# Optimization experiments

Measured on AMD Instinct MI355X. Metric: run time of the kernel, lower is better.

Reference implementation:

```python
import jax, jax.numpy as jnp
import numpy as np
from jax import lax

NUM_WORD, NUM_TAG, EMB, HID, SEQ = 50000, 50, 500, 200, 4096
START, END = 48, 49
NEG = -10000.0


def setup_inputs() -> dict:
    key = jax.random.key(0)
    ks = jax.random.split(key, 16)
    s = 0.1  # weight scale for numerical sanity
    trans = jax.random.normal(ks[13], (NUM_TAG, NUM_TAG), jnp.float32)
    trans = trans.at[START, :].set(NEG).at[:, END].set(NEG)
    return {
        'sentence_ids': jax.random.randint(ks[0], (1, SEQ), 0, NUM_WORD),
        'tags_ids': jax.random.randint(ks[1], (SEQ,), 0, START),
        'embedding': jax.random.normal(ks[2], (NUM_WORD, EMB), jnp.float32),
        'w_ih_f': s * jax.random.normal(ks[3], (4 * HID, EMB), jnp.float32),
        'w_hh_f': s * jax.random.normal(ks[4], (4 * HID, HID), jnp.float32),
        'b_ih_f': s * jax.random.normal(ks[5], (4 * HID,), jnp.float32),
        'b_hh_f': s * jax.random.normal(ks[6], (4 * HID,), jnp.float32),
        'w_ih_b': s * jax.random.normal(ks[7], (4 * HID, EMB), jnp.float32),
        'w_hh_b': s * jax.random.normal(ks[8], (4 * HID, HID), jnp.float32),
        'b_ih_b': s * jax.random.normal(ks[9], (4 * HID,), jnp.float32),
        'b_hh_b': s * jax.random.normal(ks[10], (4 * HID,), jnp.float32),
        'linear_w': s * jax.random.normal(ks[11], (NUM_TAG, 2 * HID), jnp.float32),
        'linear_b': s * jax.random.normal(ks[12], (NUM_TAG,), jnp.float32),
        'transitions': trans,
        'h0': jax.random.normal(ks[14], (2, HID), jnp.float32),
        'c0': jax.random.normal(ks[15], (2, HID), jnp.float32),
    }


def _lstm_dir(x_proj, w_hh, h0, c0):
    # x_proj: [S, 4H] precomputed input projection (+ both biases)
    def step(carry, xp):
        h, c = carry
        g = xp + h @ w_hh.T  # [4H], torch gate order i,f,g,o
        i, f, gg, o = jnp.split(g, 4)
        c = jax.nn.sigmoid(f) * c + jax.nn.sigmoid(i) * jnp.tanh(gg)
        h = jax.nn.sigmoid(o) * jnp.tanh(c)
        return (h, c), h
    _, hs = lax.scan(step, (h0, c0), x_proj)
    return hs  # [S, H]


def _get_feats(sentence_ids, embedding, w_ih_f, w_hh_f, b_ih_f, b_hh_f,
               w_ih_b, w_hh_b, b_ih_b, b_hh_b, linear_w, linear_b, h0, c0):
    x = embedding[sentence_ids[0]]  # [S, EMB]
    xf = x @ w_ih_f.T + (b_ih_f + b_hh_f)  # one big GEMM, fold hh-bias in
    xb = x[::-1] @ w_ih_b.T + (b_ih_b + b_hh_b)
    hf = _lstm_dir(xf, w_hh_f, h0[0], c0[0])          # [S, H]
    hb = _lstm_dir(xb, w_hh_b, h0[1], c0[1])[::-1]    # [S, H]
    h = jnp.concatenate([hf, hb], axis=-1)            # [S, 2H]
    return h @ linear_w.T + linear_b                   # [S, NUM_TAG]


def _crf_forward(feats, transitions):
    alpha = jnp.full((NUM_TAG,), NEG, feats.dtype).at[START].set(0.0)
    def step(alpha, feat):
        smat = alpha[:, None] + transitions + feat[None, :]  # [T, T]
        return jax.nn.logsumexp(smat, axis=0), None
    alpha, _ = lax.scan(step, alpha, feats)
    return jax.nn.logsumexp(alpha + transitions[:, END])


def _gold_score(feats, tags_ids, transitions):
    tags = jnp.concatenate([jnp.array([START], tags_ids.dtype), tags_ids])
    trans_sc = transitions[tags[:-1], tags[1:]].sum()
    emit_sc = feats[jnp.arange(feats.shape[0]), tags[1:]].sum()
    return trans_sc + emit_sc + transitions[tags[-1], END]


def _viterbi(feats, transitions):
    alpha = jnp.full((NUM_TAG,), NEG, feats.dtype).at[START].set(0.0)
    def step(alpha, feat):
        smat = alpha[:, None] + feat[None, :] + transitions  # [T, T]
        return smat.max(axis=0), smat.argmax(axis=0)
    alpha, bp = lax.scan(step, alpha, feats)  # bp: [S, T]
    fin = alpha + transitions[:, END]
    best = jnp.argmax(fin)
    def bt(tag, bp_t):
        prev = bp_t[tag]
        return prev, prev
    _, prevs = lax.scan(bt, best, bp[1:][::-1])  # skip first frame, as torch
    path = jnp.concatenate([prevs[::-1], best[None]])  # [S]
    return fin[best], path


def reference(sentence_ids, tags_ids, embedding, w_ih_f, w_hh_f, b_ih_f, b_hh_f,
              w_ih_b, w_hh_b, b_ih_b, b_hh_b, linear_w, linear_b, transitions,
              h0, c0):
    feats = _get_feats(sentence_ids, embedding, w_ih_f, w_hh_f, b_ih_f, b_hh_f,
                       w_ih_b, w_hh_b, b_ih_b, b_hh_b, linear_w, linear_b, h0, c0)
    fwd_score = _crf_forward(feats, transitions)
    gold = _gold_score(feats, tags_ids, transitions)
    _, tag_seq = _viterbi(feats, transitions)
    loss = jnp.reshape(fwd_score - gold, (1,))
    return (tag_seq, loss)
```

## Files before the change

### kernel.cpp

```cpp
#include <hip/hip_runtime.h>

typedef unsigned int u32;
typedef unsigned char u8;

#define TSTART 48
#define TEND   49
#define NEGV  -10000.0f

#define O_XG     0ull
#define O_WIHF   4194304ull
#define O_WIHB   5013504ull
#define O_WHHF   5832704ull
#define O_WHHB   6193152ull
#define O_BSF    6553600ull
#define O_BSB    6556800ull
#define O_LWP    6560000ull
#define O_XF     6600000ull
#define O_XB     19707200ull
#define O_HT     32814400ull
#define O_FEATS  36091200ull
#define O_BP     36910400ull
#define O_FMAP   37115200ull
#define O_BTAG   37118400ull
#define O_SCAL   37118656ull

typedef _Float16 h2 __attribute__((ext_vector_type(2)));

__device__ __forceinline__ float fdot2(u32 a, u32 b, float c) {
#if defined(__HIP_DEVICE_COMPILE__) && __has_builtin(__builtin_amdgcn_fdot2)
    return __builtin_amdgcn_fdot2(__builtin_bit_cast(h2, a), __builtin_bit_cast(h2, b), c, false);
#else
    float d;
    asm("v_dot2_f32_f16 %0, %1, %2, %3" : "=v"(d) : "v"(a), "v"(b), "v"(c));
    return d;
#endif
}

__device__ __forceinline__ u32 pack2(float a, float b) {
    u32 lo = __builtin_bit_cast(unsigned short, (_Float16)a);
    u32 hi = __builtin_bit_cast(unsigned short, (_Float16)b);
    return lo | (hi << 16);
}

__device__ __forceinline__ float sigf(float x) { return 1.f / (1.f + __expf(-x)); }
__device__ __forceinline__ float tanhf_(float x) { return 2.f / (1.f + __expf(-2.f * x)) - 1.f; }

#define PA_END   90112
#define PB_END   180224
#define PC_END   385024
#define PD_END   589824
#define PE_END   1638400
#define PF_END   1648400
#define PG_END   1649200
#define PH_END   1650000

__global__ __launch_bounds__(256) void k_prep(
    const int* __restrict__ ids, const float* __restrict__ emb,
    const float* __restrict__ wihf, const float* __restrict__ wihb,
    const float* __restrict__ whhf, const float* __restrict__ whhb,
    const float* __restrict__ bihf, const float* __restrict__ bhhf,
    const float* __restrict__ bihb, const float* __restrict__ bhhb,
    const float* __restrict__ lw,
    u32* __restrict__ xg, u32* __restrict__ wif16, u32* __restrict__ wib16,
    u32* __restrict__ whf16, u32* __restrict__ whb16, u32* __restrict__ lwp,
    float* __restrict__ bsf, float* __restrict__ bsb)
{
    int idx = blockIdx.x * 256 + threadIdx.x;
    if (idx < PB_END) {
        int dirb = (idx >= PA_END);
        int i = idx - (dirb ? PA_END : 0);
        const float* whh = dirb ? whhb : whhf;
        u32* dst = dirb ? whb16 : whf16;
        int chunk = i / 176, off = i % 176;
        int rgrp = chunk >> 2, ks = chunk & 3;
        u32 v = 0;
        if (off < 175) {
            int m, kd;
            if (off < 168) { int q = off >> 2, e = off & 3; kd = ks * 25 + (q / 7) * 4 + e; m = q % 7; }
            else           { m = off - 168; kd = ks * 25 + 24; }
            int row = rgrp * 7 + m;
            if (row < 800) v = pack2(whh[row * 200 + 2 * kd], whh[row * 200 + 2 * kd + 1]);
        }
        dst[i] = v;
    } else if (idx < PD_END) {
        int dirb = (idx >= PC_END);
        int i = idx - (dirb ? PC_END : PB_END);
        const float* wih = dirb ? wihb : wihf;
        u32* dst = dirb ? wib16 : wif16;
        int r = i >> 8, d = i & 255;
        dst[i] = (d < 250) ? pack2(wih[r * 500 + 2 * d], wih[r * 500 + 2 * d + 1]) : 0u;
    } else if (idx < PE_END) {
        int i = idx - PD_END; int s = i >> 8, d = i & 255;
        long id = ids[s];
        xg[i] = (d < 250) ? pack2(emb[id * 500 + 2 * d], emb[id * 500 + 2 * d + 1]) : 0u;
    } else if (idx < PF_END) {
        int i = idx - PE_END; int tag = i / 200, u = i % 200;
        lwp[i] = pack2(lw[tag * 400 + 2 * u], lw[tag * 400 + 2 * u + 1]);
    } else if (idx < PG_END) {
        int j = idx - PF_END; bsf[j] = bihf[j] + bhhf[j];
    } else if (idx < PH_END) {
        int j = idx - PG_END; bsb[j] = bihb[j] + bhhb[j];
    }
}

__global__ __launch_bounds__(256, 2) void k_gemm(
    const u32* __restrict__ xg, const u32* __restrict__ wf, const u32* __restrict__ wb,
    const float* __restrict__ bsf, const float* __restrict__ bsb,
    float* __restrict__ xf, float* __restrict__ xb)
{
    int z = blockIdx.z;
    const u32* W = z ? wb : wf;
    const float* bs = z ? bsb : bsf;
    float* out = z ? xb : xf;
    int m0 = blockIdx.x * 256, n0 = blockIdx.y * 128;
    int t = threadIdx.x;

    __shared__ u32 As[16][256];
    __shared__ u32 Bs[16][128];

    float acc[16][8];
#pragma unroll
    for (int m = 0; m < 16; m++)
#pragma unroll
        for (int n = 0; n < 8; n++) acc[m][n] = 0.f;

    int arow = m0 + t; if (z) arow = 4095 - arow;
    const u32* aptr = xg + (size_t)arow * 256;
    int bj = n0 + (t >> 1);
    int ko = (t & 1) * 8;
    const u32* bptr = W + (size_t)bj * 256 + ko;

    int ry = t >> 4, cx = t & 15;

    for (int kc = 0; kc < 16; ++kc) {
        int kd = kc * 16;
        uint4 a0 = *(const uint4*)(aptr + kd);
        uint4 a1 = *(const uint4*)(aptr + kd + 4);
        uint4 a2 = *(const uint4*)(aptr + kd + 8);
        uint4 a3 = *(const uint4*)(aptr + kd + 12);
        uint4 bv0 = {0,0,0,0}, bv1 = {0,0,0,0};
        if (bj < 800) { bv0 = *(const uint4*)(bptr + kd); bv1 = *(const uint4*)(bptr + kd + 4); }
        __syncthreads();
        u32 ad[16] = {a0.x,a0.y,a0.z,a0.w, a1.x,a1.y,a1.z,a1.w,
                      a2.x,a2.y,a2.z,a2.w, a3.x,a3.y,a3.z,a3.w};
#pragma unroll
        for (int i = 0; i < 16; i++) As[i][t] = ad[i];
        u32 bd[8] = {bv0.x,bv0.y,bv0.z,bv0.w, bv1.x,bv1.y,bv1.z,bv1.w};
#pragma unroll
        for (int i = 0; i < 8; i++) Bs[ko + i][t >> 1] = bd[i];
        __syncthreads();
#pragma unroll
        for (int d = 0; d < 16; ++d) {
            const u32* ar = &As[d][ry * 16];
            uint4 x0 = *(const uint4*)(ar);
            uint4 x1 = *(const uint4*)(ar + 4);
            uint4 x2 = *(const uint4*)(ar + 8);
            uint4 x3 = *(const uint4*)(ar + 12);
            const u32* br = &Bs[d][cx * 8];
            uint4 y0 = *(const uint4*)(br);
            uint4 y1 = *(const uint4*)(br + 4);
            u32 am[16] = {x0.x,x0.y,x0.z,x0.w, x1.x,x1.y,x1.z,x1.w,
                          x2.x,x2.y,x2.z,x2.w, x3.x,x3.y,x3.z,x3.w};
            u32 bn[8] = {y0.x,y0.y,y0.z,y0.w, y1.x,y1.y,y1.z,y1.w};
#pragma unroll
            for (int m = 0; m < 16; m++)
#pragma unroll
                for (int n = 0; n < 8; n++)
                    acc[m][n] = fdot2(am[m], bn[n], acc[m][n]);
        }
    }
    int col = n0 + cx * 8;
    if (col < 800) {
        float4 bi0 = *(const float4*)(bs + col);
        float4 bi1 = *(const float4*)(bs + col + 4);
#pragma unroll
        for (int m = 0; m < 16; m++) {
            size_t ro = (size_t)(m0 + ry * 16 + m) * 800 + col;
            float4 o0 = {acc[m][0]+bi0.x, acc[m][1]+bi0.y, acc[m][2]+bi0.z, acc[m][3]+bi0.w};
            float4 o1 = {acc[m][4]+bi1.x, acc[m][5]+bi1.y, acc[m][6]+bi1.z, acc[m][7]+bi1.w};
            *(float4*)(out + ro) = o0;
            *(float4*)(out + ro + 4) = o1;
        }
    }
}


#define DOTQ(Wv, A) \
    A = fdot2(Wv.x, hb.x, A); A = fdot2(Wv.y, hb.y, A); \
    A = fdot2(Wv.z, hb.z, A); A = fdot2(Wv.w, hb.w, A);

#define DOT_LDS_ROW(off, A) { uint4 w = *(const uint4*)(wl + (off)); DOTQ(w, A) }

#define REDUCE(A) A += __shfl_xor(A, 1); A += __shfl_xor(A, 2);

__global__ __launch_bounds__(512)
void k_lstm(
    const u32* __restrict__ whf, const u32* __restrict__ whb,
    const float* __restrict__ xf, const float* __restrict__ xb,
    const float* __restrict__ h0, const float* __restrict__ c0,
    u32* __restrict__ hallT)
{
    int dir = blockIdx.x, t = threadIdx.x;
    const u32* Wh = dir ? whb : whf;
    const float* xp = dir ? xb : xf;
    int ks = t & 3, rgrp = t >> 2, r0 = rgrp * 7;

    __shared__ __align__(16) u32 wlds[512 * 76];
    __shared__ __align__(16) u32 hsh[112];
    __shared__ float gsh[800];
    __shared__ u32 hstage[800];

    const uint4* p = (const uint4*)(Wh + (size_t)t * 176);
    u32* wl = wlds + t * 76;
#pragma unroll
    for (int i = 0; i < 19; ++i) *(uint4*)(wl + i * 4) = p[i];

    uint4 R0  = p[19], R1  = p[20];
    uint4 R2  = p[21], R3  = p[22], R4  = p[23], R5  = p[24], R6  = p[25], R7  = p[26], R8  = p[27];
    uint4 R9  = p[28], R10 = p[29], R11 = p[30], R12 = p[31], R13 = p[32], R14 = p[33], R15 = p[34];
    uint4 R16 = p[35], R17 = p[36], R18 = p[37], R19 = p[38], R20 = p[39], R21 = p[40], R22 = p[41];
    const u32* p1 = Wh + (size_t)t * 176 + 168;
    u32 U0 = p1[0], U1 = p1[1], U2 = p1[2], U3 = p1[3], U4 = p1[4], U5 = p1[5], U6 = p1[6];

    if (t < 112) hsh[t] = 0u;
    __syncthreads();

    float cst = 0.f;
    int haddr = 0;
    if (t < 200) {
        cst = c0[dir * 200 + t];
        int u = t >> 1;
        haddr = (u / 25) * 28 + (u % 25);
        if (!(t & 1)) hsh[haddr] = pack2(h0[dir * 200 + t], h0[dir * 200 + t + 1]);
    }
    __syncthreads();

    const u32* hbase = hsh + ks * 28;

    for (int s = 0; s < 4096; ++s) {
        float xr0 = 0.f, xr1 = 0.f, xr2 = 0.f, xr3 = 0.f;
        if (t < 200) {
            size_t xo = (size_t)s * 800 + t;
            xr0 = xp[xo]; xr1 = xp[xo + 200]; xr2 = xp[xo + 400]; xr3 = xp[xo + 600];
        }
        if ((s & 7) == 0 && s && t < 100) {
            int s0 = s - 8;
            u32 a0 = hstage[t],       a1 = hstage[100 + t], a2 = hstage[200 + t], a3 = hstage[300 + t];
            u32 a4 = hstage[400 + t], a5 = hstage[500 + t], a6 = hstage[600 + t], a7 = hstage[700 + t];
            uint4* dst;
            uint4 v0, v1;
            if (dir == 0) {
                dst = (uint4*)(hallT + (size_t)t * 4096 + s0);
                v0 = (uint4){a0, a1, a2, a3}; v1 = (uint4){a4, a5, a6, a7};
            } else {
                dst = (uint4*)(hallT + (size_t)(100 + t) * 4096 + (4088 - s0));
                v0 = (uint4){a7, a6, a5, a4}; v1 = (uint4){a3, a2, a1, a0};
            }
            dst[0] = v0; dst[1] = v1;
        }

        float acc0 = 0.f, acc1 = 0.f, acc2 = 0.f, acc3 = 0.f, acc4 = 0.f, acc5 = 0.f, acc6 = 0.f;
        {
            uint4 hb = *(const uint4*)(hbase + 0);
            DOT_LDS_ROW(0,  acc0) DOT_LDS_ROW(4,  acc1) DOT_LDS_ROW(8,  acc2)
            DOT_LDS_ROW(12, acc3) DOT_LDS_ROW(16, acc4) DOT_LDS_ROW(20, acc5)
            DOT_LDS_ROW(24, acc6)
        }
        {
            uint4 hb = *(const uint4*)(hbase + 12);
            DOTQ(R2, acc0) DOTQ(R3, acc1) DOTQ(R4, acc2) DOTQ(R5, acc3)
            DOTQ(R6, acc4) DOTQ(R7, acc5) DOTQ(R8, acc6)
        }
        {
            uint4 hb = *(const uint4*)(hbase + 4);
            DOT_LDS_ROW(28, acc0) DOT_LDS_ROW(32, acc1) DOT_LDS_ROW(36, acc2)
            DOT_LDS_ROW(40, acc3) DOT_LDS_ROW(44, acc4) DOT_LDS_ROW(48, acc5)
            DOT_LDS_ROW(52, acc6)
        }
        {
            uint4 hb = *(const uint4*)(hbase + 16);
            DOTQ(R9,  acc0) DOTQ(R10, acc1) DOTQ(R11, acc2) DOTQ(R12, acc3)
            DOTQ(R13, acc4) DOTQ(R14, acc5) DOTQ(R15, acc6)
        }
        {
            uint4 hb = *(const uint4*)(hbase + 8);
            DOT_LDS_ROW(56, acc0) DOT_LDS_ROW(60, acc1) DOT_LDS_ROW(64, acc2)
            DOT_LDS_ROW(68, acc3) DOT_LDS_ROW(72, acc4)
            DOTQ(R0, acc5) DOTQ(R1, acc6)
        }
        {
            uint4 hb = *(const uint4*)(hbase + 20);
            DOTQ(R16, acc0) DOTQ(R17, acc1) DOTQ(R18, acc2) DOTQ(R19, acc3)
            DOTQ(R20, acc4) DOTQ(R21, acc5) DOTQ(R22, acc6)
        }
        {
            u32 hb1 = hbase[24];
            acc0 = fdot2(U0, hb1, acc0); acc1 = fdot2(U1, hb1, acc1);
            acc2 = fdot2(U2, hb1, acc2); acc3 = fdot2(U3, hb1, acc3);
            acc4 = fdot2(U4, hb1, acc4); acc5 = fdot2(U5, hb1, acc5);
            acc6 = fdot2(U6, hb1, acc6);
        }
        REDUCE(acc0) REDUCE(acc1) REDUCE(acc2) REDUCE(acc3) REDUCE(acc4) REDUCE(acc5) REDUCE(acc6)
        if (ks == 0 && r0 < 800) {
            gsh[r0] = acc0;
            if (r0 + 1 < 800) gsh[r0 + 1] = acc1;
            if (r0 + 2 < 800) gsh[r0 + 2] = acc2;
            if (r0 + 3 < 800) gsh[r0 + 3] = acc3;
            if (r0 + 4 < 800) gsh[r0 + 4] = acc4;
            if (r0 + 5 < 800) gsh[r0 + 5] = acc5;
            if (r0 + 6 < 800) gsh[r0 + 6] = acc6;
        }
        __syncthreads();

        if (t < 200) {
            float gi = gsh[t] + xr0, gf = gsh[200 + t] + xr1;
            float gg = gsh[400 + t] + xr2, go = gsh[600 + t] + xr3;
            float is = sigf(gi), fs = sigf(gf), gt = tanhf_(gg), os = sigf(go);
            cst = fs * cst + is * gt;
            float hv = os * tanhf_(cst);
            float hq = __shfl_xor(hv, 1);
            if (!(t & 1)) {
                u32 pv = pack2(hv, hq);
                hsh[haddr] = pv;
                hstage[(s & 7) * 100 + (t >> 1)] = pv;
            }
        }
        __syncthreads();
    }
    if (t < 100) {
        u32 a0 = hstage[t],       a1 = hstage[100 + t], a2 = hstage[200 + t], a3 = hstage[300 + t];
        u32 a4 = hstage[400 + t], a5 = hstage[500 + t], a6 = hstage[600 + t], a7 = hstage[700 + t];
        uint4* dst;
        uint4 v0, v1;
        if (dir == 0) {
            dst = (uint4*)(hallT + (size_t)t * 4096 + 4088);
            v0 = (uint4){a0, a1, a2, a3}; v1 = (uint4){a4, a5, a6, a7};
        } else {
            dst = (uint4*)(hallT + (size_t)(100 + t) * 4096);
            v0 = (uint4){a7, a6, a5, a4}; v1 = (uint4){a3, a2, a1, a0};
        }
        dst[0] = v0; dst[1] = v1;
    }
}

__global__ __launch_bounds__(64) void k_linear(
    const u32* __restrict__ hallT, const u32* __restrict__ lwp,
    const float* __restrict__ lb, float* __restrict__ feats)
{
    int s = blockIdx.x, t = threadIdx.x;
    __shared__ __align__(16) u32 hc[200];
#pragma unroll
    for (int k = 0; k < 4; k++) {
        int u = t + 64 * k;
        if (u < 200) hc[u] = hallT[(size_t)u * 4096 + s];
    }
    __syncthreads();
    if (t < 50) {
        const uint4* wp = (const uint4*)(lwp + t * 200);
        const uint4* hp = (const uint4*)hc;
        float acc = lb[t];
#pragma unroll 10
        for (int c = 0; c < 50; c++) {
            uint4 wv = wp[c]; uint4 hv = hp[c];
            acc = fdot2(wv.x, hv.x, acc); acc = fdot2(wv.y, hv.y, acc);
            acc = fdot2(wv.z, hv.z, acc); acc = fdot2(wv.w, hv.w, acc);
        }
        feats[(size_t)s * 50 + t] = acc;
    }
}

__global__ __launch_bounds__(512) void k_crf(
    const float* __restrict__ feats, const float* __restrict__ trans,
    const int* __restrict__ tags, u8* __restrict__ bp, float* __restrict__ scal)
{
    __shared__ float tl[2500];
    __shared__ float al[2][64];
    __shared__ float red[512];
    int t = threadIdx.x;
    for (int i = t; i < 2500; i += 512) tl[i] = trans[i];
    __syncthreads();

    int role = blockIdx.x;
    if (role == 2) {
        float loc = 0.f;
        for (int i = t; i < 4096; i += 512) {
            int prev = i ? tags[i - 1] : TSTART;
            int cur = tags[i];
            loc += tl[prev * 50 + cur] + feats[(size_t)i * 50 + cur];
        }
        red[t] = loc; __syncthreads();
        for (int w = 256; w > 0; w >>= 1) { if (t < w) red[t] += red[t + w]; __syncthreads(); }
        if (t == 0) scal[1] = red[0] + tl[tags[4095] * 50 + TEND];
        return;
    }

    int j = t >> 3, q = t & 7;
    bool jv = j < 50;
    float Tc[7];
#pragma unroll
    for (int r = 0; r < 7; r++) {
        int i = q + 8 * r;
        Tc[r] = (jv && i < 50) ? tl[i * 50 + j] : 0.f;
    }
    if (t < 64) al[0][t] = (t == TSTART) ? 0.f : NEGV;
    __syncthreads();

    int cur = 0;
    float fcur = 0.f;
    if (q == 0 && jv) fcur = feats[j];

    if (role == 0) {
        for (int s = 0; s < 4096; ++s) {
            float fnext = 0.f;
            if (s + 1 < 4096 && q == 0 && jv) fnext = feats[(size_t)(s + 1) * 50 + j];
            float v[7]; float m = -3.0e38f;
#pragma unroll
            for (int r = 0; r < 7; r++) {
                int i = q + 8 * r;
                float vv = (i < 50) ? al[cur][i] + Tc[r] : -3.0e38f;
                v[r] = vv; m = fmaxf(m, vv);
            }
            m = fmaxf(m, __shfl_xor(m, 1));
            m = fmaxf(m, __shfl_xor(m, 2));
            m = fmaxf(m, __shfl_xor(m, 4));
            float sum = 0.f;
#pragma unroll
            for (int r = 0; r < 7; r++) {
                int i = q + 8 * r;
                if (i < 50) sum += __expf(v[r] - m);
            }
            sum += __shfl_xor(sum, 1);
            sum += __shfl_xor(sum, 2);
            sum += __shfl_xor(sum, 4);
            if (q == 0 && jv) al[cur ^ 1][j] = fcur + m + __logf(sum);
            fcur = fnext; cur ^= 1;
            __syncthreads();
        }
        if (t == 0) {
            float m = -3.0e38f;
            for (int i = 0; i < 50; i++) m = fmaxf(m, al[cur][i] + tl[i * 50 + TEND]);
            float sm = 0.f;
            for (int i = 0; i < 50; i++) sm += __expf(al[cur][i] + tl[i * 50 + TEND] - m);
            scal[0] = m + __logf(sm);
        }
    } else {
        for (int s = 0; s < 4096; ++s) {
            float fnext = 0.f;
            if (s + 1 < 4096 && q == 0 && jv) fnext = feats[(size_t)(s + 1) * 50 + j];
            float m = -3.0e38f; int mi = 63;
#pragma unroll
            for (int r = 0; r < 7; r++) {
                int i = q + 8 * r;
                float vv = (i < 50) ? al[cur][i] + Tc[r] : -3.0e38f;
                if (vv > m) { m = vv; mi = i; }
            }
#pragma unroll
            for (int k = 1; k < 8; k <<= 1) {
                float om = __shfl_xor(m, k); int oi = __shfl_xor(mi, k);
                if (om > m || (om == m && oi < mi)) { m = om; mi = oi; }
            }
            if (q == 0 && jv) {
                al[cur ^ 1][j] = m + fcur;
                bp[(size_t)s * 50 + j] = (u8)mi;
            }
            fcur = fnext; cur ^= 1;
            __syncthreads();
        }
        if (t == 0) {
            float best = -3.0e38f; int bi = 0;
            for (int i = 0; i < 50; i++) {
                float f = al[cur][i] + tl[i * 50 + TEND];
                if (f > best) { best = f; bi = i; }
            }
            ((int*)scal)[2] = bi;
        }
    }
}

__global__ __launch_bounds__(64) void k_maps(const u8* __restrict__ bp, u8* __restrict__ fmap)
{
    __shared__ __align__(4) u8 bpl[3200];
    int c = blockIdx.x, t = threadIdx.x;
    const u32* src = (const u32*)(bp + (size_t)c * 3200);
    u32* dst = (u32*)bpl;
    for (int i = t; i < 800; i += 64) dst[i] = src[i];
    __syncthreads();
    if (t < 50) {
        int y = t;
        for (int k = 63; k >= 0; --k) y = bpl[k * 50 + y];
        fmap[c * 50 + t] = (u8)y;
    }
}

__global__ __launch_bounds__(64) void k_chase(const u8* __restrict__ fmap, const float* __restrict__ scal,
                                              u8* __restrict__ btag, float* __restrict__ dout)
{
    __shared__ __align__(4) u8 fl[3200];
    int t = threadIdx.x;
    for (int i = t; i < 800; i += 64) ((u32*)fl)[i] = ((const u32*)fmap)[i];
    __syncthreads();
    if (t == 0) {
        int b = ((const int*)scal)[2];
        btag[63] = (u8)b;
        for (int c = 63; c >= 1; --c) { b = fl[c * 50 + b]; btag[c - 1] = (u8)b; }
        dout[4096] = scal[0] - scal[1];
    }
}

__global__ __launch_bounds__(64) void k_replay(const u8* __restrict__ bp, const u8* __restrict__ btag,
                                               float* __restrict__ dout)
{
    __shared__ __align__(4) u8 bpl[3200];
    int c = blockIdx.x, t = threadIdx.x;
    for (int i = t; i < 800; i += 64) ((u32*)bpl)[i] = ((const u32*)(bp + (size_t)c * 3200))[i];
    __syncthreads();
    if (t == 0) {
        int y = btag[c];
        dout[c * 64 + 63] = (float)y;
        for (int k = 62; k >= 0; --k) {
            y = bpl[(k + 1) * 50 + y];
            dout[c * 64 + k] = (float)y;
        }
    }
}

extern "C" void kernel_launch(void* const* d_in, const int* in_sizes, int n_in,
                              void* d_out, int out_size, void* d_ws, size_t ws_size,
                              hipStream_t stream)
{
    const int*   ids   = (const int*)d_in[0];
    const int*   tags  = (const int*)d_in[1];
    const float* emb   = (const float*)d_in[2];
    const float* wihf  = (const float*)d_in[3];
    const float* whhf  = (const float*)d_in[4];
    const float* bihf  = (const float*)d_in[5];
    const float* bhhf  = (const float*)d_in[6];
    const float* wihb  = (const float*)d_in[7];
    const float* whhb  = (const float*)d_in[8];
    const float* bihb  = (const float*)d_in[9];
    const float* bhhb  = (const float*)d_in[10];
    const float* lw    = (const float*)d_in[11];
    const float* lb    = (const float*)d_in[12];
    const float* trans = (const float*)d_in[13];
    const float* h0    = (const float*)d_in[14];
    const float* c0    = (const float*)d_in[15];
    float* dout = (float*)d_out;

    char* w = (char*)d_ws;
    u32*   xg    = (u32*)(w + O_XG);
    u32*   wif16 = (u32*)(w + O_WIHF);
    u32*   wib16 = (u32*)(w + O_WIHB);
    u32*   whf16 = (u32*)(w + O_WHHF);
    u32*   whb16 = (u32*)(w + O_WHHB);
    float* bsf   = (float*)(w + O_BSF);
    float* bsb   = (float*)(w + O_BSB);
    u32*   lwp   = (u32*)(w + O_LWP);
    float* xf    = (float*)(w + O_XF);
    float* xb    = (float*)(w + O_XB);
    u32*   hallT = (u32*)(w + O_HT);
    float* feats = (float*)(w + O_FEATS);
    u8*    bp    = (u8*)(w + O_BP);
    u8*    fmap  = (u8*)(w + O_FMAP);
    u8*    btag  = (u8*)(w + O_BTAG);
    float* scal  = (float*)(w + O_SCAL);

    k_prep<<<6446, 256, 0, stream>>>(ids, emb, wihf, wihb, whhf, whhb,
                                     bihf, bhhf, bihb, bhhb, lw,
                                     xg, wif16, wib16, whf16, whb16, lwp, bsf, bsb);
    k_gemm<<<dim3(16, 7, 2), 256, 0, stream>>>(xg, wif16, wib16, bsf, bsb, xf, xb);
    k_lstm<<<2, 512, 0, stream>>>(whf16, whb16, xf, xb, h0, c0, hallT);
    k_linear<<<4096, 64, 0, stream>>>(hallT, lwp, lb, feats);
    k_crf<<<3, 512, 0, stream>>>(feats, trans, tags, bp, scal);
    k_maps<<<64, 64, 0, stream>>>(bp, fmap);
    k_chase<<<1, 64, 0, stream>>>(fmap, scal, btag, dout);
    k_replay<<<64, 64, 0, stream>>>(bp, btag, dout);
}
```

Measured before the change: 8.528 ms.

## Pin part of recurrent weights via inline asm loads, stream rest from global each step

Only 11 of the per-thread register-resident weight vectors (plus the tail) are now loaded once through inline-asm global loads, which the compiler cannot rematerialise. The remaining 12 vectors are re-read from global memory (L1/L2) on every timestep, and the dot-product order is rearranged to hide that load latency. The intent is to cut VGPR pressure and avoid spills or compiler rematerialisation in the 512-thread LSTM kernel. The cost is added per-step global load traffic and latency inside the serial recurrence.

```diff
diff --git a/kernel.cpp b/kernel.cpp
--- a/kernel.cpp
+++ b/kernel.cpp
@@ -2,6 +2,7 @@
 
 typedef unsigned int u32;
 typedef unsigned char u8;
+typedef u32 u32x4 __attribute__((ext_vector_type(4)));
 
 #define TSTART 48
 #define TEND   49
@@ -185,6 +186,11 @@
 }
 
 
+#define GLOADW(dst, ptr, off) \
+    asm volatile("global_load_dwordx4 %0, %1, off offset:" #off "\n\t" \
+                 "s_waitcnt vmcnt(0)" \
+                 : "=&v"(dst) : "v"(ptr) : "memory")
+
 #define DOTQ(Wv, A) \
     A = fdot2(Wv.x, hb.x, A); A = fdot2(Wv.y, hb.y, A); \
     A = fdot2(Wv.z, hb.z, A); A = fdot2(Wv.w, hb.w, A);
@@ -215,12 +221,13 @@
 #pragma unroll
     for (int i = 0; i < 19; ++i) *(uint4*)(wl + i * 4) = p[i];
 
-    uint4 R0  = p[19], R1  = p[20];
-    uint4 R2  = p[21], R3  = p[22], R4  = p[23], R5  = p[24], R6  = p[25], R7  = p[26], R8  = p[27];
-    uint4 R9  = p[28], R10 = p[29], R11 = p[30], R12 = p[31], R13 = p[32], R14 = p[33], R15 = p[34];
-    uint4 R16 = p[35], R17 = p[36], R18 = p[37], R19 = p[38], R20 = p[39], R21 = p[40], R22 = p[41];
-    const u32* p1 = Wh + (size_t)t * 176 + 168;
-    u32 U0 = p1[0], U1 = p1[1], U2 = p1[2], U3 = p1[3], U4 = p1[4], U5 = p1[5], U6 = p1[6];
+    const u32* wptr = Wh + (size_t)t * 176;
+    u32x4 RA0,RA1,RA2,RA3,RA4,RA5,RA6,RA7,RA8,RA9,RA10, U01, U23;
+    GLOADW(RA0,  wptr, 304); GLOADW(RA1,  wptr, 320); GLOADW(RA2,  wptr, 336);
+    GLOADW(RA3,  wptr, 352); GLOADW(RA4,  wptr, 368); GLOADW(RA5,  wptr, 384);
+    GLOADW(RA6,  wptr, 400); GLOADW(RA7,  wptr, 416); GLOADW(RA8,  wptr, 432);
+    GLOADW(RA9,  wptr, 448); GLOADW(RA10, wptr, 464);
+    GLOADW(U01,  wptr, 672); GLOADW(U23,  wptr, 688);
 
     if (t < 112) hsh[t] = 0u;
     __syncthreads();
@@ -238,6 +245,8 @@
     const u32* hbase = hsh + ks * 28;
 
     for (int s = 0; s < 4096; ++s) {
+        uint4 SE0 = p[30], SE1 = p[31], SE2 = p[32], SE3 = p[33], SE4 = p[34];
+
         float xr0 = 0.f, xr1 = 0.f, xr2 = 0.f, xr3 = 0.f;
         if (t < 200) {
             size_t xo = (size_t)s * 800 + t;
@@ -267,11 +276,6 @@
             DOT_LDS_ROW(24, acc6)
         }
         {
-            uint4 hb = *(const uint4*)(hbase + 12);
-            DOTQ(R2, acc0) DOTQ(R3, acc1) DOTQ(R4, acc2) DOTQ(R5, acc3)
-            DOTQ(R6, acc4) DOTQ(R7, acc5) DOTQ(R8, acc6)
-        }
-        {
             uint4 hb = *(const uint4*)(hbase + 4);
             DOT_LDS_ROW(28, acc0) DOT_LDS_ROW(32, acc1) DOT_LDS_ROW(36, acc2)
             DOT_LDS_ROW(40, acc3) DOT_LDS_ROW(44, acc4) DOT_LDS_ROW(48, acc5)
@@ -279,26 +283,32 @@
         }
         {
             uint4 hb = *(const uint4*)(hbase + 16);
-            DOTQ(R9,  acc0) DOTQ(R10, acc1) DOTQ(R11, acc2) DOTQ(R12, acc3)
-            DOTQ(R13, acc4) DOTQ(R14, acc5) DOTQ(R15, acc6)
-        }
+            DOTQ(RA9, acc0) DOTQ(RA10, acc1)
+            DOTQ(SE0, acc2) DOTQ(SE1, acc3) DOTQ(SE2, acc4) DOTQ(SE3, acc5) DOTQ(SE4, acc6)
+        }
+        uint4 SF0 = p[35], SF1 = p[36], SF2 = p[37], SF3 = p[38], SF4 = p[39], SF5 = p[40], SF6 = p[41];
         {
             uint4 hb = *(const uint4*)(hbase + 8);
             DOT_LDS_ROW(56, acc0) DOT_LDS_ROW(60, acc1) DOT_LDS_ROW(64, acc2)
             DOT_LDS_ROW(68, acc3) DOT_LDS_ROW(72, acc4)
-            DOTQ(R0, acc5) DOTQ(R1, acc6)
+            DOTQ(RA0, acc5) DOTQ(RA1, acc6)
+        }
+        {
+            uint4 hb = *(const uint4*)(hbase + 12);
+            DOTQ(RA2, acc0) DOTQ(RA3, acc1) DOTQ(RA4, acc2) DOTQ(RA5, acc3)
+            DOTQ(RA6, acc4) DOTQ(RA7, acc5) DOTQ(RA8, acc6)
         }
         {
             uint4 hb = *(const uint4*)(hbase + 20);
-            DOTQ(R16, acc0) DOTQ(R17, acc1) DOTQ(R18, acc2) DOTQ(R19, acc3)
-            DOTQ(R20, acc4) DOTQ(R21, acc5) DOTQ(R22, acc6)
+            DOTQ(SF0, acc0) DOTQ(SF1, acc1) DOTQ(SF2, acc2) DOTQ(SF3, acc3)
+            DOTQ(SF4, acc4) DOTQ(SF5, acc5) DOTQ(SF6, acc6)
         }
         {
             u32 hb1 = hbase[24];
-            acc0 = fdot2(U0, hb1, acc0); acc1 = fdot2(U1, hb1, acc1);
-            acc2 = fdot2(U2, hb1, acc2); acc3 = fdot2(U3, hb1, acc3);
-            acc4 = fdot2(U4, hb1, acc4); acc5 = fdot2(U5, hb1, acc5);
-            acc6 = fdot2(U6, hb1, acc6);
+            acc0 = fdot2(U01.x, hb1, acc0); acc1 = fdot2(U01.y, hb1, acc1);
+            acc2 = fdot2(U01.z, hb1, acc2); acc3 = fdot2(U01.w, hb1, acc3);
+            acc4 = fdot2(U23.x, hb1, acc4); acc5 = fdot2(U23.y, hb1, acc5);
+            acc6 = fdot2(U23.z, hb1, acc6);
         }
         REDUCE(acc0) REDUCE(acc1) REDUCE(acc2) REDUCE(acc3) REDUCE(acc4) REDUCE(acc5) REDUCE(acc6)
         if (ks == 0 && r0 < 800) {
```

Measured after the change: 11.43 ms. 34.0% more time.
